# Kernel optimization log

Measured on AMD Instinct MI355X. Metric: run time of the kernel, lower is better.

## Reference

```python
import jax, jax.numpy as jnp
import numpy as np

B, P, E, D, A, M, V, L = 128, 196, 2048, 512, 512, 512, 10000, 21


def setup_inputs() -> dict:
    key = jax.random.key(0)
    ks = jax.random.split(key, 24)
    s = 0.02
    encoder_out = jax.random.normal(ks[0], (B, P, E), jnp.float32)
    encoded_captions = jax.random.randint(ks[1], (B, L), 0, V)
    caption_lengths = jax.random.randint(ks[2], (B,), 2, L + 1).at[0].set(L)
    return {
        "encoder_out": encoder_out,
        "encoded_captions": encoded_captions,
        "caption_lengths": caption_lengths,
        "emb_table": jax.random.normal(ks[3], (V, M), jnp.float32) * s,
        "enc_att_w": jax.random.normal(ks[4], (E, A), jnp.float32) * s,
        "enc_att_b": jnp.zeros((A,), jnp.float32),
        "dec_att_w": jax.random.normal(ks[5], (D, A), jnp.float32) * s,
        "dec_att_b": jnp.zeros((A,), jnp.float32),
        "full_att_w": jax.random.normal(ks[6], (A,), jnp.float32) * s,
        "full_att_b": jnp.zeros((), jnp.float32),
        "init_h_w": jax.random.normal(ks[7], (E, D), jnp.float32) * s,
        "init_h_b": jnp.zeros((D,), jnp.float32),
        "init_c_w": jax.random.normal(ks[8], (E, D), jnp.float32) * s,
        "init_c_b": jnp.zeros((D,), jnp.float32),
        "f_beta_w": jax.random.normal(ks[9], (D, E), jnp.float32) * s,
        "f_beta_b": jnp.zeros((E,), jnp.float32),
        "lstm_w_ih": jax.random.normal(ks[10], (4 * D, M + E), jnp.float32) * s,
        "lstm_b_ih": jnp.zeros((4 * D,), jnp.float32),
        "lstm_w_hh": jax.random.normal(ks[11], (4 * D, D), jnp.float32) * s,
        "lstm_b_hh": jnp.zeros((4 * D,), jnp.float32),
        "fc_w": jax.random.normal(ks[12], (V, D), jnp.float32) * s,
        "fc_b": jnp.zeros((V,), jnp.float32),
    }


def reference(encoder_out, encoded_captions, caption_lengths, emb_table,
              enc_att_w, enc_att_b, dec_att_w, dec_att_b, full_att_w, full_att_b,
              init_h_w, init_h_b, init_c_w, init_c_b, f_beta_w, f_beta_b,
              lstm_w_ih, lstm_b_ih, lstm_w_hh, lstm_b_hh, fc_w, fc_b):
    # sort by caption length descending (as in torch)
    order = jnp.argsort(-caption_lengths)
    enc = encoder_out[order]                 # [B,P,E]
    caps = encoded_captions[order]           # [B,L]
    dec_len = caption_lengths[order] - 1     # [B]
    T = caps.shape[1] - 1

    emb_seq = emb_table[caps]                # [B,L,M]
    mean = enc.mean(axis=1)                  # [B,E]
    h0 = mean @ init_h_w + init_h_b
    c0 = mean @ init_c_w + init_c_b
    att1 = enc @ enc_att_w + enc_att_b       # [B,P,A] (hoisted: constant over t)

    def step(carry, t):
        h, c = carry
        att2 = h @ dec_att_w + dec_att_b                              # [B,A]
        e = jnp.einsum('bpa,a->bp', jax.nn.relu(att1 + att2[:, None, :]), full_att_w) + full_att_b
        alpha = jax.nn.softmax(e, axis=1)                             # [B,P]
        awe = jnp.einsum('bpe,bp->be', enc, alpha)                    # [B,E]
        gate = jax.nn.sigmoid(h @ f_beta_w + f_beta_b)                # [B,E]
        x = jnp.concatenate([emb_seq[:, t, :], gate * awe], axis=1)   # [B,M+E]
        g = x @ lstm_w_ih.T + lstm_b_ih + h @ lstm_w_hh.T + lstm_b_hh
        i, f, gg, o = jnp.split(g, 4, axis=1)
        c_new = jax.nn.sigmoid(f) * c + jax.nn.sigmoid(i) * jnp.tanh(gg)
        h_new = jax.nn.sigmoid(o) * jnp.tanh(c_new)
        pred = h_new @ fc_w.T + fc_b                                  # [B,V]
        active = (t < dec_len)[:, None]
        pred = jnp.where(active, pred, 0.0)
        alpha = jnp.where(active, alpha, 0.0)
        return (h_new, c_new), (pred, alpha)

    _, (preds, alphas) = jax.lax.scan(step, (h0, c0), jnp.arange(T))
    predictions = jnp.moveaxis(preds, 0, 1)   # [B,T,V]
    alphas = jnp.moveaxis(alphas, 0, 1)       # [B,T,P]
    return predictions, alphas
```

## Files before the change

kernel.cpp:

```cpp
#include <hip/hip_runtime.h>
#include <math.h>

#define B_ 128
#define P_ 196
#define E_ 2048
#define D_ 512
#define A_ 512
#define M_ 512
#define V_ 10000
#define L_ 21
#define T_ 20

#define NBLK_ 256
#define SLOTS_WORDS (NBLK_ * 16 + 16)

typedef __attribute__((ext_vector_type(8))) short bf16x8;
typedef __attribute__((ext_vector_type(4))) float f32x4;
typedef unsigned short ushort_t;

__global__ void order_kernel(const int* __restrict__ lens, const int* __restrict__ caps,
                             int* __restrict__ order, int* __restrict__ declen,
                             int* __restrict__ row_map, int* __restrict__ tok_rows,
                             unsigned* __restrict__ bar) {
  __shared__ int s_order[B_];
  int tid = threadIdx.x;
  for (int i = tid; i < SLOTS_WORDS; i += 256) bar[i] = 0u;
  if (tid < B_) {
    int li = lens[tid];
    int r = 0;
    for (int j = 0; j < B_; ++j) {
      int lj = lens[j];
      r += (lj > li) || (lj == li && j < tid);
    }
    s_order[r] = tid;
    declen[r] = li - 1;
  }
  __syncthreads();
  if (tid < B_) order[tid] = s_order[tid];
  for (int m = tid; m < B_ * P_; m += blockDim.x) {
    int b = m / P_, p = m - b * P_;
    row_map[m] = s_order[b] * P_ + p;
  }
  for (int i = tid; i < T_ * B_; i += blockDim.x) {
    int t = i >> 7, b = i & 127;
    tok_rows[i] = caps[s_order[b] * L_ + t];
  }
}

__global__ void mean_kernel(const float* __restrict__ enc, const int* __restrict__ order,
                            float* __restrict__ mean) {
  int b = blockIdx.y;
  int e = blockIdx.x * blockDim.x + threadIdx.x;
  int ob = order[b];
  const float* base = enc + (long long)ob * P_ * E_ + e;
  float s = 0.f;
  for (int p = 0; p < P_; ++p) s += base[(long long)p * E_];
  mean[b * E_ + e] = s * (1.0f / P_);
}

__device__ __forceinline__ unsigned f2bf_u(float f) {
  unsigned u = __float_as_uint(f);
  return (u + 0x7fffu + ((u >> 16) & 1u)) >> 16;
}
__device__ __forceinline__ float bf2f(ushort_t h) {
  return __uint_as_float(((unsigned)h) << 16);
}

__global__ void enc2bf_kernel(const float* __restrict__ enc, const int* __restrict__ row_map,
                              ushort_t* __restrict__ out) {
  int r = blockIdx.x;
  int row = row_map[r];
  const float* src = enc + (long long)row * E_ + threadIdx.x * 8;
  float4 v0 = ((const float4*)src)[0];
  float4 v1 = ((const float4*)src)[1];
  float f[8] = {v0.x, v0.y, v0.z, v0.w, v1.x, v1.y, v1.z, v1.w};
  unsigned h[8];
#pragma unroll
  for (int j = 0; j < 8; ++j) h[j] = f2bf_u(f[j]);
  int4 o;
  o.x = (int)(h[0] | (h[1] << 16));
  o.y = (int)(h[2] | (h[3] << 16));
  o.z = (int)(h[4] | (h[5] << 16));
  o.w = (int)(h[6] | (h[7] << 16));
  *(int4*)(out + (long long)r * E_ + threadIdx.x * 8) = o;
}

__global__ void transpose_kernel(const float* __restrict__ in, float* __restrict__ out,
                                 int K, int N) {
  __shared__ float tt[32][33];
  int bx = blockIdx.x * 32;
  int by = blockIdx.y * 32;
  int lx = threadIdx.x & 31, ly = threadIdx.x >> 5;
#pragma unroll
  for (int i = 0; i < 32; i += 8) tt[ly + i][lx] = in[(long long)(by + ly + i) * N + bx + lx];
  __syncthreads();
#pragma unroll
  for (int i = 0; i < 32; i += 8)
    out[(long long)(bx + ly + i) * K + by + lx] = tt[lx][ly + i];
}

__global__ __launch_bounds__(256) void gemm32_kernel(
    const float* __restrict__ A, const float* __restrict__ Bm,
    const float* __restrict__ bias, float* __restrict__ C, int M, int N, int K) {
  __shared__ float As[16][64];
  __shared__ float Bs[16][64];
  const int tid = threadIdx.x;
  const int bm = blockIdx.y * 64, bn = blockIdx.x * 64;
  const int tm = tid >> 4, tn = tid & 15;
  float acc[4][4];
#pragma unroll
  for (int i = 0; i < 4; ++i)
#pragma unroll
    for (int j = 0; j < 4; ++j) acc[i][j] = 0.f;
  const int lm = tid >> 2;
  const int lk = (tid & 3) * 4;
  for (int k0 = 0; k0 < K; k0 += 16) {
    {
      int m = bm + lm;
      float4 v = make_float4(0.f, 0.f, 0.f, 0.f);
      if (m < M) v = *(const float4*)(A + (long long)m * K + k0 + lk);
      As[lk + 0][lm] = v.x;
      As[lk + 1][lm] = v.y;
      As[lk + 2][lm] = v.z;
      As[lk + 3][lm] = v.w;
    }
    {
      int k = tid >> 4;
      int n4 = (tid & 15) * 4;
      int n = bn + n4;
      float4 v = make_float4(0.f, 0.f, 0.f, 0.f);
      if (n < N) v = *(const float4*)(Bm + (long long)(k0 + k) * N + n);
      Bs[k][n4 + 0] = v.x;
      Bs[k][n4 + 1] = v.y;
      Bs[k][n4 + 2] = v.z;
      Bs[k][n4 + 3] = v.w;
    }
    __syncthreads();
#pragma unroll
    for (int k = 0; k < 16; ++k) {
      float a0 = As[k][tm * 4 + 0], a1 = As[k][tm * 4 + 1];
      float a2 = As[k][tm * 4 + 2], a3 = As[k][tm * 4 + 3];
      float b0 = Bs[k][tn * 4 + 0], b1 = Bs[k][tn * 4 + 1];
      float b2 = Bs[k][tn * 4 + 2], b3 = Bs[k][tn * 4 + 3];
      acc[0][0] += a0 * b0; acc[0][1] += a0 * b1; acc[0][2] += a0 * b2; acc[0][3] += a0 * b3;
      acc[1][0] += a1 * b0; acc[1][1] += a1 * b1; acc[1][2] += a1 * b2; acc[1][3] += a1 * b3;
      acc[2][0] += a2 * b0; acc[2][1] += a2 * b1; acc[2][2] += a2 * b2; acc[2][3] += a2 * b3;
      acc[3][0] += a3 * b0; acc[3][1] += a3 * b1; acc[3][2] += a3 * b2; acc[3][3] += a3 * b3;
    }
    __syncthreads();
  }
#pragma unroll
  for (int i = 0; i < 4; ++i) {
    int m = bm + tm * 4 + i;
    if (m >= M) continue;
#pragma unroll
    for (int j = 0; j < 4; ++j) {
      int n = bn + tn * 4 + j;
      if (n >= N) continue;
      C[(long long)m * N + n] = acc[i][j] + (bias ? bias[n] : 0.f);
    }
  }
}

__device__ __forceinline__ void stage16(short* __restrict__ Ph, short* __restrict__ Pl,
                                        int r, int kq, float4 v0, float4 v1, float4 v2,
                                        float4 v3, bool split) {
  float f[16] = {v0.x, v0.y, v0.z, v0.w, v1.x, v1.y, v1.z, v1.w,
                 v2.x, v2.y, v2.z, v2.w, v3.x, v3.y, v3.z, v3.w};
#pragma unroll
  for (int g2 = 0; g2 < 2; ++g2) {
    int gg = (kq >> 3) + g2;
    int slot = gg ^ ((r >> 1) & 3);
    unsigned hb[8];
    float lf[8];
#pragma unroll
    for (int j = 0; j < 8; ++j) {
      float x = f[g2 * 8 + j];
      hb[j] = f2bf_u(x);
      lf[j] = x - __uint_as_float(hb[j] << 16);
    }
    int4 ph;
    ph.x = (int)(hb[0] | (hb[1] << 16));
    ph.y = (int)(hb[2] | (hb[3] << 16));
    ph.z = (int)(hb[4] | (hb[5] << 16));
    ph.w = (int)(hb[6] | (hb[7] << 16));
    *(int4*)&Ph[r * 32 + slot * 8] = ph;
    if (split) {
      unsigned lb[8];
#pragma unroll
      for (int j = 0; j < 8; ++j) lb[j] = f2bf_u(lf[j]);
      int4 pl;
      pl.x = (int)(lb[0] | (lb[1] << 16));
      pl.y = (int)(lb[2] | (lb[3] << 16));
      pl.z = (int)(lb[4] | (lb[5] << 16));
      pl.w = (int)(lb[6] | (lb[7] << 16));
      *(int4*)&Pl[r * 32 + slot * 8] = pl;
    }
  }
}

__device__ __forceinline__ void stage8(short* __restrict__ Ph, short* __restrict__ Pl,
                                       int r, int kq8, float4 v0, float4 v1) {
  int slot = kq8 ^ ((r >> 1) & 3);
  float f[8] = {v0.x, v0.y, v0.z, v0.w, v1.x, v1.y, v1.z, v1.w};
  unsigned hb[8];
  float lf[8];
#pragma unroll
  for (int j = 0; j < 8; ++j) {
    hb[j] = f2bf_u(f[j]);
    lf[j] = f[j] - __uint_as_float(hb[j] << 16);
  }
  int4 ph;
  ph.x = (int)(hb[0] | (hb[1] << 16));
  ph.y = (int)(hb[2] | (hb[3] << 16));
  ph.z = (int)(hb[4] | (hb[5] << 16));
  ph.w = (int)(hb[6] | (hb[7] << 16));
  *(int4*)&Ph[r * 32 + slot * 8] = ph;
  unsigned lb[8];
#pragma unroll
  for (int j = 0; j < 8; ++j) lb[j] = f2bf_u(lf[j]);
  int4 pl;
  pl.x = (int)(lb[0] | (lb[1] << 16));
  pl.y = (int)(lb[2] | (lb[3] << 16));
  pl.z = (int)(lb[4] | (lb[5] << 16));
  pl.w = (int)(lb[6] | (lb[7] << 16));
  *(int4*)&Pl[r * 32 + slot * 8] = pl;
}

__device__ __forceinline__ bf16x8 frag_load(const short* __restrict__ P, int row, int g) {
  int slot = g ^ ((row >> 1) & 3);
  return *(const bf16x8*)&P[row * 32 + slot * 8];
}

template <int MODE, bool SPLIT, bool SWZ, bool OB>
__global__ __launch_bounds__(256) void mfma_gemm(
    const float* __restrict__ A, int lda, const int* __restrict__ row_map,
    const float* __restrict__ Bn, int ldb,
    const float* __restrict__ bias, const float* __restrict__ bias2,
    void* __restrict__ Cv, int ldc, int M, int N, int K,
    const int* __restrict__ declen) {
  __shared__ short Ah[128 * 32];
  __shared__ short Bh[128 * 32];
  __shared__ short Al[128 * 32];
  __shared__ short Bl[128 * 32];
  const int tid = threadIdx.x;
  int bxi, byi;
  if (SWZ) {
    int gx = gridDim.x, gy = gridDim.y;
    int id = blockIdx.y * gx + blockIdx.x;
    int super = 8 * gx;
    int body = (gy & ~7) * gx;
    if (id < body) {
      int s = id / super, rem = id % super;
      byi = s * 8 + (rem & 7);
      bxi = rem >> 3;
    } else {
      int rem = id - body;
      byi = (gy & ~7) + rem / gx;
      bxi = rem % gx;
    }
  } else {
    bxi = blockIdx.x;
    byi = blockIdx.y;
  }
  const int bm = byi * 128, bn = bxi * 128;

  f32x4 acc[4][4];
#pragma unroll
  for (int i = 0; i < 4; ++i)
#pragma unroll
    for (int j = 0; j < 4; ++j) acc[i][j] = (f32x4){0.f, 0.f, 0.f, 0.f};

  const int r = tid >> 1;
  const int kq = (tid & 1) * 16;
  const int am = bm + r;
  const long long arow = row_map ? (long long)row_map[am] : (long long)am;
  const float* ap = A + arow * (long long)lda + kq;
  const int gn = bn + r;
  const float* bp = Bn + (long long)gn * ldb + kq;
  const bool bok = gn < N;

  const int lane = tid & 63;
  const int wv = tid >> 6, wr = wv >> 1, wc = wv & 1;
  const int lr = lane & 15, g = lane >> 4;

  float4 z4 = make_float4(0.f, 0.f, 0.f, 0.f);
  float4 a0 = *(const float4*)(ap), a1 = *(const float4*)(ap + 4);
  float4 a2 = *(const float4*)(ap + 8), a3 = *(const float4*)(ap + 12);
  float4 b0 = bok ? *(const float4*)(bp) : z4;
  float4 b1 = bok ? *(const float4*)(bp + 4) : z4;
  float4 b2 = bok ? *(const float4*)(bp + 8) : z4;
  float4 b3 = bok ? *(const float4*)(bp + 12) : z4;

  for (int k0 = 0; k0 < K; k0 += 32) {
    stage16(Ah, Al, r, kq, a0, a1, a2, a3, SPLIT);
    stage16(Bh, Bl, r, kq, b0, b1, b2, b3, SPLIT);
    __syncthreads();
    if (k0 + 32 < K) {
      int kn = k0 + 32;
      a0 = *(const float4*)(ap + kn);
      a1 = *(const float4*)(ap + kn + 4);
      a2 = *(const float4*)(ap + kn + 8);
      a3 = *(const float4*)(ap + kn + 12);
      b0 = bok ? *(const float4*)(bp + kn) : z4;
      b1 = bok ? *(const float4*)(bp + kn + 4) : z4;
      b2 = bok ? *(const float4*)(bp + kn + 8) : z4;
      b3 = bok ? *(const float4*)(bp + kn + 12) : z4;
    }
    bf16x8 ah[4], bh[4];
#pragma unroll
    for (int i = 0; i < 4; ++i) {
      ah[i] = frag_load(Ah, wr * 64 + i * 16 + lr, g);
      bh[i] = frag_load(Bh, wc * 64 + i * 16 + lr, g);
    }
#pragma unroll
    for (int i = 0; i < 4; ++i)
#pragma unroll
      for (int j = 0; j < 4; ++j)
        acc[i][j] = __builtin_amdgcn_mfma_f32_16x16x32_bf16(ah[i], bh[j], acc[i][j], 0, 0, 0);
    if (SPLIT) {
      bf16x8 al2[4], bl2[4];
#pragma unroll
      for (int i = 0; i < 4; ++i) {
        al2[i] = frag_load(Al, wr * 64 + i * 16 + lr, g);
        bl2[i] = frag_load(Bl, wc * 64 + i * 16 + lr, g);
      }
#pragma unroll
      for (int i = 0; i < 4; ++i)
#pragma unroll
        for (int j = 0; j < 4; ++j)
          acc[i][j] = __builtin_amdgcn_mfma_f32_16x16x32_bf16(al2[i], bh[j], acc[i][j], 0, 0, 0);
#pragma unroll
      for (int i = 0; i < 4; ++i)
#pragma unroll
        for (int j = 0; j < 4; ++j)
          acc[i][j] = __builtin_amdgcn_mfma_f32_16x16x32_bf16(ah[i], bl2[j], acc[i][j], 0, 0, 0);
    }
    __syncthreads();
  }

#pragma unroll
  for (int j = 0; j < 4; ++j) {
    int n = bn + wc * 64 + j * 16 + lr;
    float bj = 0.f;
    if (n < N) {
      if (bias) bj += bias[n];
      if (bias2) bj += bias2[n];
    }
#pragma unroll
    for (int i = 0; i < 4; ++i) {
#pragma unroll
      for (int rr = 0; rr < 4; ++rr) {
        int m = bm + wr * 64 + i * 16 + g * 4 + rr;
        float v = acc[i][j][rr] + bj;
        if (MODE == 0) {
          if (OB)
            ((ushort_t*)Cv)[(long long)m * ldc + n] = (ushort_t)f2bf_u(v);
          else
            ((float*)Cv)[(long long)m * ldc + n] = v;
        } else {
          if (n < N) {
            int b = m & 127, t = m >> 7;
            ((float*)Cv)[(long long)b * (T_ * V_) + (long long)t * V_ + n] =
                (t < declen[b]) ? v : 0.f;
          }
        }
      }
    }
  }
}

__device__ __forceinline__ void mfma_tile64(
    const float* __restrict__ ap, const float* __restrict__ bp, int K,
    f32x4 (&acc)[2][2], short* Ah, short* Al, short* Bh, short* Bl,
    int sr, int skq, int wr, int wc, int lr, int g) {
  float4 a0 = *(const float4*)(ap), a1 = *(const float4*)(ap + 4);
  float4 b0 = *(const float4*)(bp), b1 = *(const float4*)(bp + 4);
  for (int k0 = 0; k0 < K; k0 += 32) {
    stage8(Ah, Al, sr, skq, a0, a1);
    stage8(Bh, Bl, sr, skq, b0, b1);
    __syncthreads();
    if (k0 + 32 < K) {
      a0 = *(const float4*)(ap + k0 + 32);
      a1 = *(const float4*)(ap + k0 + 36);
      b0 = *(const float4*)(bp + k0 + 32);
      b1 = *(const float4*)(bp + k0 + 36);
    }
    bf16x8 fah[2], fbh[2], fal[2], fbl[2];
#pragma unroll
    for (int i = 0; i < 2; ++i) {
      fah[i] = frag_load(Ah, wr * 32 + i * 16 + lr, g);
      fal[i] = frag_load(Al, wr * 32 + i * 16 + lr, g);
      fbh[i] = frag_load(Bh, wc * 32 + i * 16 + lr, g);
      fbl[i] = frag_load(Bl, wc * 32 + i * 16 + lr, g);
    }
#pragma unroll
    for (int i = 0; i < 2; ++i)
#pragma unroll
      for (int j = 0; j < 2; ++j) {
        acc[i][j] = __builtin_amdgcn_mfma_f32_16x16x32_bf16(fah[i], fbh[j], acc[i][j], 0, 0, 0);
        acc[i][j] = __builtin_amdgcn_mfma_f32_16x16x32_bf16(fal[i], fbh[j], acc[i][j], 0, 0, 0);
        acc[i][j] = __builtin_amdgcn_mfma_f32_16x16x32_bf16(fah[i], fbl[j], acc[i][j], 0, 0, 0);
      }
    __syncthreads();
  }
}

__device__ __forceinline__ void gsync(unsigned* __restrict__ slots, unsigned target) {
  __syncthreads();
  if (threadIdx.x == 0) {
    __threadfence();
    __hip_atomic_store(&slots[blockIdx.x * 16], target, __ATOMIC_RELEASE,
                       __HIP_MEMORY_SCOPE_AGENT);
  }
  if (threadIdx.x < 64) {
#pragma unroll
    for (int k = 0; k < 4; ++k) {
      unsigned idx = ((unsigned)threadIdx.x * 4 + k) * 16;
      while (__hip_atomic_load(&slots[idx], __ATOMIC_ACQUIRE, __HIP_MEMORY_SCOPE_AGENT) <
             target) {
        __builtin_amdgcn_s_sleep(2);
      }
    }
    __threadfence();
  }
  __syncthreads();
}

template <bool ENCBF>
__global__ __launch_bounds__(256, 1) void loop_kernel(
    const float* __restrict__ att1f, const ushort_t* __restrict__ att1b,
    const float* __restrict__ encf, const ushort_t* __restrict__ encb,
    const int* __restrict__ order, const int* __restrict__ declen,
    const float* __restrict__ decT, const float* __restrict__ decb,
    const float* __restrict__ fbT, const float* __restrict__ fbb,
    const float* __restrict__ whh, const float* __restrict__ wih,
    const float* __restrict__ faw, const float* __restrict__ fab,
    const float* __restrict__ g_all, float* __restrict__ g_part,
    float* __restrict__ gh, float* __restrict__ h_all, float* __restrict__ c,
    float* __restrict__ xh, float* __restrict__ gate, float* __restrict__ att2,
    float* __restrict__ alphas_out, unsigned* __restrict__ bar) {
  __shared__ short Ah[64 * 32];
  __shared__ short Bh[64 * 32];
  __shared__ short Al[64 * 32];
  __shared__ short Bl[64 * 32];
  __shared__ float att2_s[512];
  __shared__ float w_s[512];
  __shared__ float e_s[P_];
  __shared__ float red[8];

  unsigned* slots = bar;
  unsigned tgt = 0;

  const int bid = blockIdx.x, tid = threadIdx.x;
  const int lane = tid & 63, wv = tid >> 6, wr = wv >> 1, wc = wv & 1;
  const int lr = lane & 15, g = lane >> 4;
  const int sr = tid >> 2, skq = tid & 3;

  const float fb0 = fab[0];
  float wr8[8];
  if (ENCBF) {
    const float4* wp = (const float4*)(faw + lane * 8);
#pragma unroll
    for (int q = 0; q < 2; ++q) {
      float4 v = wp[q];
      wr8[q * 4 + 0] = v.x;
      wr8[q * 4 + 1] = v.y;
      wr8[q * 4 + 2] = v.z;
      wr8[q * 4 + 3] = v.w;
    }
  }

  for (int t = 0; t < T_; ++t) {
    const float* h_cur = h_all + t * (B_ * D_);
    if (bid < 144) {
      int nt = bid % 72, mt = bid / 72;
      int bn = nt * 64;
      const float* Bb;
      if (bn < 512) Bb = decT + bn * 512;
      else if (bn < 2560) Bb = fbT + (bn - 512) * 512;
      else Bb = whh + (bn - 2560) * 512;
      f32x4 acc[2][2];
#pragma unroll
      for (int i = 0; i < 2; ++i)
#pragma unroll
        for (int j = 0; j < 2; ++j) acc[i][j] = (f32x4){0.f, 0.f, 0.f, 0.f};
      mfma_tile64(h_cur + (mt * 64 + sr) * 512 + skq * 8, Bb + sr * 512 + skq * 8, 512,
                  acc, Ah, Al, Bh, Bl, sr, skq, wr, wc, lr, g);
#pragma unroll
      for (int j = 0; j < 2; ++j) {
        int n = bn + wc * 32 + j * 16 + lr;
#pragma unroll
        for (int i = 0; i < 2; ++i) {
#pragma unroll
          for (int rr = 0; rr < 4; ++rr) {
            int m = mt * 64 + wr * 32 + i * 16 + g * 4 + rr;
            float v = acc[i][j][rr];
            if (bn < 512) {
              att2[m * 512 + n] = v + decb[n];
            } else if (bn < 2560) {
              int nc = n - 512;
              gate[m * 2048 + nc] = 1.f / (1.f + __expf(-(v + fbb[nc])));
            } else {
              gh[m * 2048 + (n - 2560)] = v;
            }
          }
        }
      }
    }
    gsync(slots, ++tgt);
    {
      const int b = bid & 127, half = bid >> 7;
      if (ENCBF) {
        float a2r[8];
        const float4* a2p = (const float4*)(att2 + b * 512 + lane * 8);
#pragma unroll
        for (int q = 0; q < 2; ++q) {
          float4 v = a2p[q];
          a2r[q * 4 + 0] = v.x;
          a2r[q * 4 + 1] = v.y;
          a2r[q * 4 + 2] = v.z;
          a2r[q * 4 + 3] = v.w;
        }
        const ushort_t* a1base = att1b + (long long)b * P_ * 512 + lane * 8;
        const bf16x8 zv = (bf16x8)(short)0;
        for (int p0 = wv; p0 < P_; p0 += 16) {
          int pA = p0, pB = p0 + 4, pC = p0 + 8, pD = p0 + 12;
          bf16x8 hA = (pA < P_) ? *(const bf16x8*)(a1base + (long long)pA * 512) : zv;
          bf16x8 hB = (pB < P_) ? *(const bf16x8*)(a1base + (long long)pB * 512) : zv;
          bf16x8 hC = (pC < P_) ? *(const bf16x8*)(a1base + (long long)pC * 512) : zv;
          bf16x8 hD = (pD < P_) ? *(const bf16x8*)(a1base + (long long)pD * 512) : zv;
          float sA = 0.f, sB = 0.f, sC = 0.f, sD = 0.f;
#pragma unroll
          for (int j = 0; j < 8; ++j) {
            float xA = bf2f((ushort_t)hA[j]) + a2r[j];
            float xB = bf2f((ushort_t)hB[j]) + a2r[j];
            float xC = bf2f((ushort_t)hC[j]) + a2r[j];
            float xD = bf2f((ushort_t)hD[j]) + a2r[j];
            sA += (xA > 0.f ? xA : 0.f) * wr8[j];
            sB += (xB > 0.f ? xB : 0.f) * wr8[j];
            sC += (xC > 0.f ? xC : 0.f) * wr8[j];
            sD += (xD > 0.f ? xD : 0.f) * wr8[j];
          }
#pragma unroll
          for (int off = 32; off; off >>= 1) {
            sA += __shfl_down(sA, off);
            sB += __shfl_down(sB, off);
            sC += __shfl_down(sC, off);
            sD += __shfl_down(sD, off);
          }
          if (lane == 0) {
            e_s[pA] = sA + fb0;
            if (pB < P_) e_s[pB] = sB + fb0;
            if (pC < P_) e_s[pC] = sC + fb0;
            if (pD < P_) e_s[pD] = sD + fb0;
          }
        }
      } else {
        for (int i = tid; i < 512; i += 256) {
          att2_s[i] = att2[b * 512 + i];
          w_s[i] = faw[i];
        }
        __syncthreads();
        for (int p = wv; p < P_; p += 4) {
          const float* row = att1f + ((long long)b * P_ + p) * 512;
          float s = 0.f;
#pragma unroll
          for (int i2 = 0; i2 < 8; ++i2) {
            int ix = lane + i2 * 64;
            float v = row[ix] + att2_s[ix];
            s += (v > 0.f ? v : 0.f) * w_s[ix];
          }
          for (int off = 32; off; off >>= 1) s += __shfl_down(s, off);
          if (lane == 0) e_s[p] = s + fb0;
        }
      }
      __syncthreads();
      float mx = -1e30f;
      for (int p = tid; p < P_; p += 256) mx = fmaxf(mx, e_s[p]);
      for (int off = 32; off; off >>= 1) mx = fmaxf(mx, __shfl_down(mx, off));
      if (lane == 0) red[wv] = mx;
      __syncthreads();
      mx = fmaxf(fmaxf(red[0], red[1]), fmaxf(red[2], red[3]));
      float ssum = 0.f;
      for (int p = tid; p < P_; p += 256) {
        float ev = __expf(e_s[p] - mx);
        e_s[p] = ev;
        ssum += ev;
      }
      for (int off = 32; off; off >>= 1) ssum += __shfl_down(ssum, off);
      if (lane == 0) red[4 + wv] = ssum;
      __syncthreads();
      float inv = 1.f / (red[4] + red[5] + red[6] + red[7]);
      const bool active = (t < declen[b]);
      for (int p = tid; p < P_; p += 256) {
        float al = e_s[p] * inv;
        e_s[p] = al;
        if (half == 0)
          alphas_out[(long long)b * (T_ * P_) + t * P_ + p] = active ? al : 0.f;
      }
      __syncthreads();
      if (ENCBF) {
        const ushort_t* ebc = encb + (long long)b * (P_ * E_) + half * 1024 + tid * 4;
        int col = half * 1024 + tid * 4;
        float s0 = 0.f, s1 = 0.f, s2 = 0.f, s3 = 0.f;
        short4 buf0, buf1, buf2, buf3, buf4, buf5, buf6, buf7;
        buf0 = *(const short4*)(ebc + 0LL * E_);
        buf1 = *(const short4*)(ebc + 1LL * E_);
        buf2 = *(const short4*)(ebc + 2LL * E_);
        buf3 = *(const short4*)(ebc + 3LL * E_);
        buf4 = *(const short4*)(ebc + 4LL * E_);
        buf5 = *(const short4*)(ebc + 5LL * E_);
        buf6 = *(const short4*)(ebc + 6LL * E_);
        buf7 = *(const short4*)(ebc + 7LL * E_);
        for (int p0 = 0; p0 < 184; p0 += 8) {
          short4 c0 = buf0, c1 = buf1, c2 = buf2, c3 = buf3;
          short4 c4 = buf4, c5 = buf5, c6 = buf6, c7 = buf7;
          const ushort_t* nb = ebc + (long long)(p0 + 8) * E_;
          buf0 = *(const short4*)(nb + 0LL * E_);
          buf1 = *(const short4*)(nb + 1LL * E_);
          buf2 = *(const short4*)(nb + 2LL * E_);
          buf3 = *(const short4*)(nb + 3LL * E_);
          buf4 = *(const short4*)(nb + 4LL * E_);
          buf5 = *(const short4*)(nb + 5LL * E_);
          buf6 = *(const short4*)(nb + 6LL * E_);
          buf7 = *(const short4*)(nb + 7LL * E_);
          float a;
          a = e_s[p0 + 0]; s0 += a * bf2f((ushort_t)c0.x); s1 += a * bf2f((ushort_t)c0.y); s2 += a * bf2f((ushort_t)c0.z); s3 += a * bf2f((ushort_t)c0.w);
          a = e_s[p0 + 1]; s0 += a * bf2f((ushort_t)c1.x); s1 += a * bf2f((ushort_t)c1.y); s2 += a * bf2f((ushort_t)c1.z); s3 += a * bf2f((ushort_t)c1.w);
          a = e_s[p0 + 2]; s0 += a * bf2f((ushort_t)c2.x); s1 += a * bf2f((ushort_t)c2.y); s2 += a * bf2f((ushort_t)c2.z); s3 += a * bf2f((ushort_t)c2.w);
          a = e_s[p0 + 3]; s0 += a * bf2f((ushort_t)c3.x); s1 += a * bf2f((ushort_t)c3.y); s2 += a * bf2f((ushort_t)c3.z); s3 += a * bf2f((ushort_t)c3.w);
          a = e_s[p0 + 4]; s0 += a * bf2f((ushort_t)c4.x); s1 += a * bf2f((ushort_t)c4.y); s2 += a * bf2f((ushort_t)c4.z); s3 += a * bf2f((ushort_t)c4.w);
          a = e_s[p0 + 5]; s0 += a * bf2f((ushort_t)c5.x); s1 += a * bf2f((ushort_t)c5.y); s2 += a * bf2f((ushort_t)c5.z); s3 += a * bf2f((ushort_t)c5.w);
          a = e_s[p0 + 6]; s0 += a * bf2f((ushort_t)c6.x); s1 += a * bf2f((ushort_t)c6.y); s2 += a * bf2f((ushort_t)c6.z); s3 += a * bf2f((ushort_t)c6.w);
          a = e_s[p0 + 7]; s0 += a * bf2f((ushort_t)c7.x); s1 += a * bf2f((ushort_t)c7.y); s2 += a * bf2f((ushort_t)c7.z); s3 += a * bf2f((ushort_t)c7.w);
        }
        {
          float a;
          a = e_s[184]; s0 += a * bf2f((ushort_t)buf0.x); s1 += a * bf2f((ushort_t)buf0.y); s2 += a * bf2f((ushort_t)buf0.z); s3 += a * bf2f((ushort_t)buf0.w);
          a = e_s[185]; s0 += a * bf2f((ushort_t)buf1.x); s1 += a * bf2f((ushort_t)buf1.y); s2 += a * bf2f((ushort_t)buf1.z); s3 += a * bf2f((ushort_t)buf1.w);
          a = e_s[186]; s0 += a * bf2f((ushort_t)buf2.x); s1 += a * bf2f((ushort_t)buf2.y); s2 += a * bf2f((ushort_t)buf2.z); s3 += a * bf2f((ushort_t)buf2.w);
          a = e_s[187]; s0 += a * bf2f((ushort_t)buf3.x); s1 += a * bf2f((ushort_t)buf3.y); s2 += a * bf2f((ushort_t)buf3.z); s3 += a * bf2f((ushort_t)buf3.w);
          a = e_s[188]; s0 += a * bf2f((ushort_t)buf4.x); s1 += a * bf2f((ushort_t)buf4.y); s2 += a * bf2f((ushort_t)buf4.z); s3 += a * bf2f((ushort_t)buf4.w);
          a = e_s[189]; s0 += a * bf2f((ushort_t)buf5.x); s1 += a * bf2f((ushort_t)buf5.y); s2 += a * bf2f((ushort_t)buf5.z); s3 += a * bf2f((ushort_t)buf5.w);
          a = e_s[190]; s0 += a * bf2f((ushort_t)buf6.x); s1 += a * bf2f((ushort_t)buf6.y); s2 += a * bf2f((ushort_t)buf6.z); s3 += a * bf2f((ushort_t)buf6.w);
          a = e_s[191]; s0 += a * bf2f((ushort_t)buf7.x); s1 += a * bf2f((ushort_t)buf7.y); s2 += a * bf2f((ushort_t)buf7.z); s3 += a * bf2f((ushort_t)buf7.w);
          short4 t0 = *(const short4*)(ebc + 192LL * E_);
          short4 t1 = *(const short4*)(ebc + 193LL * E_);
          short4 t2 = *(const short4*)(ebc + 194LL * E_);
          short4 t3 = *(const short4*)(ebc + 195LL * E_);
          a = e_s[192]; s0 += a * bf2f((ushort_t)t0.x); s1 += a * bf2f((ushort_t)t0.y); s2 += a * bf2f((ushort_t)t0.z); s3 += a * bf2f((ushort_t)t0.w);
          a = e_s[193]; s0 += a * bf2f((ushort_t)t1.x); s1 += a * bf2f((ushort_t)t1.y); s2 += a * bf2f((ushort_t)t1.z); s3 += a * bf2f((ushort_t)t1.w);
          a = e_s[194]; s0 += a * bf2f((ushort_t)t2.x); s1 += a * bf2f((ushort_t)t2.y); s2 += a * bf2f((ushort_t)t2.z); s3 += a * bf2f((ushort_t)t2.w);
          a = e_s[195]; s0 += a * bf2f((ushort_t)t3.x); s1 += a * bf2f((ushort_t)t3.y); s2 += a * bf2f((ushort_t)t3.z); s3 += a * bf2f((ushort_t)t3.w);
        }
        float4 gv = *(const float4*)(gate + b * 2048 + col);
        float4 o;
        o.x = gv.x * s0;
        o.y = gv.y * s1;
        o.z = gv.z * s2;
        o.w = gv.w * s3;
        *(float4*)(xh + b * 2048 + col) = o;
      } else {
        const int ob = order[b];
        const float* eb = encf + (long long)ob * (P_ * E_);
        for (int e0 = half * 1024 + tid; e0 < half * 1024 + 1024; e0 += 256) {
          float s2 = 0.f;
#pragma unroll 4
          for (int p = 0; p < P_; ++p) s2 += e_s[p] * eb[p * 2048 + e0];
          xh[b * 2048 + e0] = gate[b * 2048 + e0] * s2;
        }
      }
    }
    gsync(slots, ++tgt);
    {
      int kc = bid >> 6, rem = bid & 63, mt = rem >> 5, nt = rem & 31;
      int bn = nt * 64;
      f32x4 acc[2][2];
#pragma unroll
      for (int i = 0; i < 2; ++i)
#pragma unroll
        for (int j = 0; j < 2; ++j) acc[i][j] = (f32x4){0.f, 0.f, 0.f, 0.f};
      mfma_tile64(xh + (mt * 64 + sr) * 2048 + kc * 512 + skq * 8,
                  wih + (long long)(bn + sr) * 2560 + 512 + kc * 512 + skq * 8, 512,
                  acc, Ah, Al, Bh, Bl, sr, skq, wr, wc, lr, g);
      float* gp = g_part + kc * (128 * 2048);
#pragma unroll
      for (int j = 0; j < 2; ++j) {
        int n = bn + wc * 32 + j * 16 + lr;
#pragma unroll
        for (int i = 0; i < 2; ++i) {
#pragma unroll
          for (int rr = 0; rr < 4; ++rr) {
            int m = mt * 64 + wr * 32 + i * 16 + g * 4 + rr;
            gp[m * 2048 + n] = acc[i][j][rr];
          }
        }
      }
    }
    gsync(slots, ++tgt);
    {
      int idx = bid * 256 + tid;
      int b = idx >> 9, d = idx & 511;
      int base = b * 2048 + d;
      const float* ge = g_all + (long long)t * (128 * 2048);
      float gi = ge[base] + gh[base];
      float gf2 = ge[base + 512] + gh[base + 512];
      float gg2 = ge[base + 1024] + gh[base + 1024];
      float go = ge[base + 1536] + gh[base + 1536];
#pragma unroll
      for (int kc = 0; kc < 4; ++kc) {
        const float* gp = g_part + kc * (128 * 2048) + base;
        gi += gp[0];
        gf2 += gp[512];
        gg2 += gp[1024];
        go += gp[1536];
      }
      float si = 1.f / (1.f + __expf(-gi));
      float sf = 1.f / (1.f + __expf(-gf2));
      float so = 1.f / (1.f + __expf(-go));
      float cn = sf * c[idx] + si * tanhf(gg2);
      float hn = so * tanhf(cn);
      c[idx] = cn;
      h_all[(t + 1) * (B_ * D_) + idx] = hn;
    }
    gsync(slots, ++tgt);
  }
}

extern "C" void kernel_launch(void* const* d_in, const int* in_sizes, int n_in,
                              void* d_out, int out_size, void* d_ws, size_t ws_size,
                              hipStream_t stream) {
  const float* enc       = (const float*)d_in[0];
  const int*   caps      = (const int*)d_in[1];
  const int*   lens      = (const int*)d_in[2];
  const float* emb       = (const float*)d_in[3];
  const float* enc_att_w = (const float*)d_in[4];
  const float* enc_att_b = (const float*)d_in[5];
  const float* dec_att_w = (const float*)d_in[6];
  const float* dec_att_b = (const float*)d_in[7];
  const float* full_att_w = (const float*)d_in[8];
  const float* full_att_b = (const float*)d_in[9];
  const float* init_h_w  = (const float*)d_in[10];
  const float* init_h_b  = (const float*)d_in[11];
  const float* init_c_w  = (const float*)d_in[12];
  const float* init_c_b  = (const float*)d_in[13];
  const float* f_beta_w  = (const float*)d_in[14];
  const float* f_beta_b  = (const float*)d_in[15];
  const float* lstm_w_ih = (const float*)d_in[16];
  const float* lstm_b_ih = (const float*)d_in[17];
  const float* lstm_w_hh = (const float*)d_in[18];
  const float* lstm_b_hh = (const float*)d_in[19];
  const float* fc_w      = (const float*)d_in[20];
  const float* fc_b      = (const float*)d_in[21];

  float* out = (float*)d_out;
  float* alphas_out = out + (long long)B_ * T_ * V_;

  float* g_all    = out;
  float* g_part   = out + 6 * 1024 * 1024;
  float* encattwT = out + 8 * 1024 * 1024;
  float* decT     = out + 9 * 1024 * 1024 + 512 * 1024;
  float* fbT      = decT + 512 * 512;
  float* gh       = out + 12 * 1024 * 1024;

  size_t cur = 0;
  char* wsb = (char*)d_ws;
  auto alloc = [&](size_t bytes) {
    size_t off = cur;
    cur = (cur + bytes + 255) & ~(size_t)255;
    return (void*)(wsb + off);
  };
  const size_t ATT1B_BYTES = (size_t)B_ * P_ * A_ * 2;
  const size_t ENCB_BYTES  = (size_t)B_ * P_ * E_ * 2;
  const size_t ATT1F_BYTES = (size_t)B_ * P_ * A_ * 4;
  const size_t REST_BYTES  = (size_t)(B_ * E_ + (T_ + 1) * B_ * D_ + B_ * D_ + B_ * A_ +
                                      B_ * E_ + B_ * E_) * 4 +
                             (2 * B_ + B_ * P_ + T_ * B_ + SLOTS_WORDS + 64) * 4 + 4096;
  const bool bfpath = ws_size >= ATT1B_BYTES + ENCB_BYTES + REST_BYTES + (1u << 20);

  ushort_t* att1b = nullptr;
  ushort_t* encbf = nullptr;
  float* att1f = nullptr;
  if (bfpath) {
    att1b = (ushort_t*)alloc(ATT1B_BYTES);
    encbf = (ushort_t*)alloc(ENCB_BYTES);
  } else {
    att1f = (float*)alloc(ATT1F_BYTES);
  }
  float* mean  = (float*)alloc((size_t)B_ * E_ * 4);
  float* h_all = (float*)alloc((size_t)(T_ + 1) * B_ * D_ * 4);
  float* c     = (float*)alloc((size_t)B_ * D_ * 4);
  float* att2  = (float*)alloc((size_t)B_ * A_ * 4);
  float* gate  = (float*)alloc((size_t)B_ * E_ * 4);
  float* xh    = (float*)alloc((size_t)B_ * E_ * 4);
  int* order   = (int*)alloc(B_ * 4);
  int* declen  = (int*)alloc(B_ * 4);
  int* row_map = (int*)alloc((size_t)B_ * P_ * 4);
  int* tok_rows = (int*)alloc((size_t)T_ * B_ * 4);
  unsigned* bar = (unsigned*)alloc(SLOTS_WORDS * 4);

  hipLaunchKernelGGL(order_kernel, dim3(1), dim3(256), 0, stream, lens, caps, order, declen,
                     row_map, tok_rows, bar);
  hipLaunchKernelGGL(transpose_kernel, dim3(16, 64), dim3(256), 0, stream, enc_att_w,
                     encattwT, E_, A_);
  hipLaunchKernelGGL(transpose_kernel, dim3(16, 16), dim3(256), 0, stream, dec_att_w, decT,
                     D_, A_);
  hipLaunchKernelGGL(transpose_kernel, dim3(64, 16), dim3(256), 0, stream, f_beta_w, fbT,
                     D_, E_);
  hipLaunchKernelGGL(mean_kernel, dim3(E_ / 256, B_), dim3(256), 0, stream, enc, order, mean);
  hipLaunchKernelGGL(gemm32_kernel, dim3(D_ / 64, 2), dim3(256), 0, stream, mean, init_h_w,
                     init_h_b, h_all, B_, D_, E_);
  hipLaunchKernelGGL(gemm32_kernel, dim3(D_ / 64, 2), dim3(256), 0, stream, mean, init_c_w,
                     init_c_b, c, B_, D_, E_);
  if (bfpath) {
    hipLaunchKernelGGL((mfma_gemm<0, false, true, true>), dim3(A_ / 128, (B_ * P_) / 128),
                       dim3(256), 0, stream, enc, E_, row_map, encattwT, E_, enc_att_b,
                       (const float*)nullptr, (void*)att1b, A_, B_ * P_, A_, E_,
                       (const int*)nullptr);
    hipLaunchKernelGGL(enc2bf_kernel, dim3(B_ * P_), dim3(256), 0, stream, enc, row_map,
                       encbf);
  } else {
    hipLaunchKernelGGL((mfma_gemm<0, false, true, false>), dim3(A_ / 128, (B_ * P_) / 128),
                       dim3(256), 0, stream, enc, E_, row_map, encattwT, E_, enc_att_b,
                       (const float*)nullptr, (void*)att1f, A_, B_ * P_, A_, E_,
                       (const int*)nullptr);
  }
  hipLaunchKernelGGL((mfma_gemm<0, true, false, false>), dim3((4 * D_) / 128, (T_ * B_) / 128),
                     dim3(256), 0, stream, emb, M_, tok_rows, lstm_w_ih, M_ + E_, lstm_b_ih,
                     lstm_b_hh, (void*)g_all, 4 * D_, T_ * B_, 4 * D_, M_,
                     (const int*)nullptr);
  if (bfpath) {
    hipLaunchKernelGGL((loop_kernel<true>), dim3(NBLK_), dim3(256), 0, stream,
                       (const float*)nullptr, att1b, (const float*)nullptr, encbf, order,
                       declen, decT, dec_att_b, fbT, f_beta_b, lstm_w_hh, lstm_w_ih,
                       full_att_w, full_att_b, g_all, g_part, gh, h_all, c, xh, gate, att2,
                       alphas_out, bar);
  } else {
    hipLaunchKernelGGL((loop_kernel<false>), dim3(NBLK_), dim3(256), 0, stream, att1f,
                       (const ushort_t*)nullptr, enc, (const ushort_t*)nullptr, order,
                       declen, decT, dec_att_b, fbT, f_beta_b, lstm_w_hh, lstm_w_ih,
                       full_att_w, full_att_b, g_all, g_part, gh, h_all, c, xh, gate, att2,
                       alphas_out, bar);
  }
  hipLaunchKernelGGL((mfma_gemm<1, true, false, false>), dim3((V_ + 127) / 128,
                     (T_ * B_) / 128), dim3(256), 0, stream, h_all + B_ * D_, D_,
                     (const int*)nullptr, fc_w, D_, fc_b, (const float*)nullptr, (void*)out,
                     V_, T_ * B_, V_, D_, declen);
}
```

Measured before the change: 5.078 ms.

## Double persistent loop grid to 512 blocks with quarter-column attention-weighted sums

```diff
diff --git a/kernel.cpp b/kernel.cpp
--- a/kernel.cpp
+++ b/kernel.cpp
@@ -11,8 +11,8 @@
 #define L_ 21
 #define T_ 20
 
-#define NBLK_ 256
-#define SLOTS_WORDS (NBLK_ * 16 + 16)
+#define NBLK_ 512
+#define SLOTS_WORDS (NBLK_ * 16 + NBLK_ * 16 + 16)
 
 typedef __attribute__((ext_vector_type(8))) short bf16x8;
 typedef __attribute__((ext_vector_type(4))) float f32x4;
@@ -415,8 +415,8 @@
   }
   if (threadIdx.x < 64) {
 #pragma unroll
-    for (int k = 0; k < 4; ++k) {
-      unsigned idx = ((unsigned)threadIdx.x * 4 + k) * 16;
+    for (int k = 0; k < NBLK_ / 64; ++k) {
+      unsigned idx = ((unsigned)threadIdx.x * (NBLK_ / 64) + k) * 16;
       while (__hip_atomic_load(&slots[idx], __ATOMIC_ACQUIRE, __HIP_MEMORY_SCOPE_AGENT) <
              target) {
         __builtin_amdgcn_s_sleep(2);
@@ -428,7 +428,7 @@
 }
 
 template <bool ENCBF>
-__global__ __launch_bounds__(256, 1) void loop_kernel(
+__global__ __launch_bounds__(256, 2) void loop_kernel(
     const float* __restrict__ att1f, const ushort_t* __restrict__ att1b,
     const float* __restrict__ encf, const ushort_t* __restrict__ encb,
     const int* __restrict__ order, const int* __restrict__ declen,
@@ -439,7 +439,8 @@
     const float* __restrict__ g_all, float* __restrict__ g_part,
     float* __restrict__ gh, float* __restrict__ h_all, float* __restrict__ c,
     float* __restrict__ xh, float* __restrict__ gate, float* __restrict__ att2,
-    float* __restrict__ alphas_out, unsigned* __restrict__ bar) {
+    float* __restrict__ alphas_out, unsigned* __restrict__ bar,
+    float* __restrict__ e_g) {
   __shared__ short Ah[64 * 32];
   __shared__ short Bh[64 * 32];
   __shared__ short Al[64 * 32];
@@ -450,6 +451,7 @@
   __shared__ float red[8];
 
   unsigned* slots = bar;
+  unsigned* pf = bar + NBLK_ * 16;
   unsigned tgt = 0;
 
   const int bid = blockIdx.x, tid = threadIdx.x;
@@ -510,165 +512,187 @@
     }
     gsync(slots, ++tgt);
     {
-      const int b = bid & 127, half = bid >> 7;
+      const int b = bid & 127, q = bid >> 7;
       if (ENCBF) {
-        float a2r[8];
-        const float4* a2p = (const float4*)(att2 + b * 512 + lane * 8);
-#pragma unroll
-        for (int q = 0; q < 2; ++q) {
-          float4 v = a2p[q];
-          a2r[q * 4 + 0] = v.x;
-          a2r[q * 4 + 1] = v.y;
-          a2r[q * 4 + 2] = v.z;
-          a2r[q * 4 + 3] = v.w;
+        if (q < 2) {
+          float a2r[8];
+          const float4* a2p = (const float4*)(att2 + b * 512 + lane * 8);
+#pragma unroll
+          for (int qq = 0; qq < 2; ++qq) {
+            float4 v = a2p[qq];
+            a2r[qq * 4 + 0] = v.x;
+            a2r[qq * 4 + 1] = v.y;
+            a2r[qq * 4 + 2] = v.z;
+            a2r[qq * 4 + 3] = v.w;
+          }
+          const ushort_t* a1base = att1b + (long long)b * P_ * 512 + lane * 8;
+          const bf16x8 zv = (bf16x8)(short)0;
+          for (int p0 = wv; p0 < P_; p0 += 16) {
+            int pA = p0, pB = p0 + 4, pC = p0 + 8, pD = p0 + 12;
+            bf16x8 hA = (pA < P_) ? *(const bf16x8*)(a1base + (long long)pA * 512) : zv;
+            bf16x8 hB = (pB < P_) ? *(const bf16x8*)(a1base + (long long)pB * 512) : zv;
+            bf16x8 hC = (pC < P_) ? *(const bf16x8*)(a1base + (long long)pC * 512) : zv;
+            bf16x8 hD = (pD < P_) ? *(const bf16x8*)(a1base + (long long)pD * 512) : zv;
+            float sA = 0.f, sB = 0.f, sC = 0.f, sD = 0.f;
+#pragma unroll
+            for (int j = 0; j < 8; ++j) {
+              float xA = bf2f((ushort_t)hA[j]) + a2r[j];
+              float xB = bf2f((ushort_t)hB[j]) + a2r[j];
+              float xC = bf2f((ushort_t)hC[j]) + a2r[j];
+              float xD = bf2f((ushort_t)hD[j]) + a2r[j];
+              sA += (xA > 0.f ? xA : 0.f) * wr8[j];
+              sB += (xB > 0.f ? xB : 0.f) * wr8[j];
+              sC += (xC > 0.f ? xC : 0.f) * wr8[j];
+              sD += (xD > 0.f ? xD : 0.f) * wr8[j];
+            }
+#pragma unroll
+            for (int off = 32; off; off >>= 1) {
+              sA += __shfl_down(sA, off);
+              sB += __shfl_down(sB, off);
+              sC += __shfl_down(sC, off);
+              sD += __shfl_down(sD, off);
+            }
+            if (lane == 0) {
+              e_s[pA] = sA + fb0;
+              if (pB < P_) e_s[pB] = sB + fb0;
+              if (pC < P_) e_s[pC] = sC + fb0;
+              if (pD < P_) e_s[pD] = sD + fb0;
+            }
+          }
+          __syncthreads();
+          float mx = -1e30f;
+          for (int p = tid; p < P_; p += 256) mx = fmaxf(mx, e_s[p]);
+          for (int off = 32; off; off >>= 1) mx = fmaxf(mx, __shfl_down(mx, off));
+          if (lane == 0) red[wv] = mx;
+          __syncthreads();
+          mx = fmaxf(fmaxf(red[0], red[1]), fmaxf(red[2], red[3]));
+          float ssum = 0.f;
+          for (int p = tid; p < P_; p += 256) {
+            float ev = __expf(e_s[p] - mx);
+            e_s[p] = ev;
+            ssum += ev;
+          }
+          for (int off = 32; off; off >>= 1) ssum += __shfl_down(ssum, off);
+          if (lane == 0) red[4 + wv] = ssum;
+          __syncthreads();
+          float inv = 1.f / (red[4] + red[5] + red[6] + red[7]);
+          const bool active = (t < declen[b]);
+          for (int p = tid; p < P_; p += 256) {
+            float al = e_s[p] * inv;
+            e_s[p] = al;
+            if (q == 0) {
+              alphas_out[(long long)b * (T_ * P_) + t * P_ + p] = active ? al : 0.f;
+              e_g[b * 256 + p] = al;
+            }
+          }
+          __syncthreads();
+          if (q == 0 && tid == 0) {
+            __threadfence();
+            __hip_atomic_store(&pf[b * 16], (unsigned)(t + 1), __ATOMIC_RELEASE,
+                               __HIP_MEMORY_SCOPE_AGENT);
+          }
+        } else {
+          if (tid == 0) {
+            while (__hip_atomic_load(&pf[b * 16], __ATOMIC_ACQUIRE,
+                                     __HIP_MEMORY_SCOPE_AGENT) < (unsigned)(t + 1)) {
+              __builtin_amdgcn_s_sleep(2);
+            }
+            __threadfence();
+          }
+          __syncthreads();
+          for (int p = tid; p < P_; p += 256) e_s[p] = e_g[b * 256 + p];
+          __syncthreads();
         }
-        const ushort_t* a1base = att1b + (long long)b * P_ * 512 + lane * 8;
-        const bf16x8 zv = (bf16x8)(short)0;
-        for (int p0 = wv; p0 < P_; p0 += 16) {
-          int pA = p0, pB = p0 + 4, pC = p0 + 8, pD = p0 + 12;
-          bf16x8 hA = (pA < P_) ? *(const bf16x8*)(a1base + (long long)pA * 512) : zv;
-          bf16x8 hB = (pB < P_) ? *(const bf16x8*)(a1base + (long long)pB * 512) : zv;
-          bf16x8 hC = (pC < P_) ? *(const bf16x8*)(a1base + (long long)pC * 512) : zv;
-          bf16x8 hD = (pD < P_) ? *(const bf16x8*)(a1base + (long long)pD * 512) : zv;
-          float sA = 0.f, sB = 0.f, sC = 0.f, sD = 0.f;
-#pragma unroll
-          for (int j = 0; j < 8; ++j) {
-            float xA = bf2f((ushort_t)hA[j]) + a2r[j];
-            float xB = bf2f((ushort_t)hB[j]) + a2r[j];
-            float xC = bf2f((ushort_t)hC[j]) + a2r[j];
-            float xD = bf2f((ushort_t)hD[j]) + a2r[j];
-            sA += (xA > 0.f ? xA : 0.f) * wr8[j];
-            sB += (xB > 0.f ? xB : 0.f) * wr8[j];
-            sC += (xC > 0.f ? xC : 0.f) * wr8[j];
-            sD += (xD > 0.f ? xD : 0.f) * wr8[j];
-          }
-#pragma unroll
-          for (int off = 32; off; off >>= 1) {
-            sA += __shfl_down(sA, off);
-            sB += __shfl_down(sB, off);
-            sC += __shfl_down(sC, off);
-            sD += __shfl_down(sD, off);
-          }
-          if (lane == 0) {
-            e_s[pA] = sA + fb0;
-            if (pB < P_) e_s[pB] = sB + fb0;
-            if (pC < P_) e_s[pC] = sC + fb0;
-            if (pD < P_) e_s[pD] = sD + fb0;
-          }
+        {
+          const int col = q * 512 + tid * 2;
+          const ushort_t* ebc = encb + (long long)b * (P_ * E_) + col;
+          float s0 = 0.f, s1 = 0.f;
+          short2 buf[14];
+#pragma unroll
+          for (int i = 0; i < 14; ++i) buf[i] = *(const short2*)(ebc + (long long)i * E_);
+          for (int ch = 0; ch < 13; ++ch) {
+            short2 cur[14];
+#pragma unroll
+            for (int i = 0; i < 14; ++i) cur[i] = buf[i];
+            const ushort_t* nb = ebc + (long long)(ch + 1) * 14 * E_;
+#pragma unroll
+            for (int i = 0; i < 14; ++i) buf[i] = *(const short2*)(nb + (long long)i * E_);
+            const float* ep = e_s + ch * 14;
+#pragma unroll
+            for (int i = 0; i < 14; ++i) {
+              float a = ep[i];
+              s0 += a * bf2f((ushort_t)cur[i].x);
+              s1 += a * bf2f((ushort_t)cur[i].y);
+            }
+          }
+          {
+            const float* ep = e_s + 182;
+#pragma unroll
+            for (int i = 0; i < 14; ++i) {
+              float a = ep[i];
+              s0 += a * bf2f((ushort_t)buf[i].x);
+              s1 += a * bf2f((ushort_t)buf[i].y);
+            }
+          }
+          float2 gv = *(const float2*)(gate + b * 2048 + col);
+          float2 o;
+          o.x = gv.x * s0;
+          o.y = gv.y * s1;
+          *(float2*)(xh + b * 2048 + col) = o;
         }
       } else {
-        for (int i = tid; i < 512; i += 256) {
-          att2_s[i] = att2[b * 512 + i];
-          w_s[i] = faw[i];
-        }
-        __syncthreads();
-        for (int p = wv; p < P_; p += 4) {
-          const float* row = att1f + ((long long)b * P_ + p) * 512;
-          float s = 0.f;
-#pragma unroll
-          for (int i2 = 0; i2 < 8; ++i2) {
-            int ix = lane + i2 * 64;
-            float v = row[ix] + att2_s[ix];
-            s += (v > 0.f ? v : 0.f) * w_s[ix];
-          }
-          for (int off = 32; off; off >>= 1) s += __shfl_down(s, off);
-          if (lane == 0) e_s[p] = s + fb0;
-        }
-      }
-      __syncthreads();
-      float mx = -1e30f;
-      for (int p = tid; p < P_; p += 256) mx = fmaxf(mx, e_s[p]);
-      for (int off = 32; off; off >>= 1) mx = fmaxf(mx, __shfl_down(mx, off));
-      if (lane == 0) red[wv] = mx;
-      __syncthreads();
-      mx = fmaxf(fmaxf(red[0], red[1]), fmaxf(red[2], red[3]));
-      float ssum = 0.f;
-      for (int p = tid; p < P_; p += 256) {
-        float ev = __expf(e_s[p] - mx);
-        e_s[p] = ev;
-        ssum += ev;
-      }
-      for (int off = 32; off; off >>= 1) ssum += __shfl_down(ssum, off);
-      if (lane == 0) red[4 + wv] = ssum;
-      __syncthreads();
-      float inv = 1.f / (red[4] + red[5] + red[6] + red[7]);
-      const bool active = (t < declen[b]);
-      for (int p = tid; p < P_; p += 256) {
-        float al = e_s[p] * inv;
-        e_s[p] = al;
-        if (half == 0)
-          alphas_out[(long long)b * (T_ * P_) + t * P_ + p] = active ? al : 0.f;
-      }
-      __syncthreads();
-      if (ENCBF) {
-        const ushort_t* ebc = encb + (long long)b * (P_ * E_) + half * 1024 + tid * 4;
-        int col = half * 1024 + tid * 4;
-        float s0 = 0.f, s1 = 0.f, s2 = 0.f, s3 = 0.f;
-        short4 buf0, buf1, buf2, buf3, buf4, buf5, buf6, buf7;
-        buf0 = *(const short4*)(ebc + 0LL * E_);
-        buf1 = *(const short4*)(ebc + 1LL * E_);
-        buf2 = *(const short4*)(ebc + 2LL * E_);
-        buf3 = *(const short4*)(ebc + 3LL * E_);
-        buf4 = *(const short4*)(ebc + 4LL * E_);
-        buf5 = *(const short4*)(ebc + 5LL * E_);
-        buf6 = *(const short4*)(ebc + 6LL * E_);
-        buf7 = *(const short4*)(ebc + 7LL * E_);
-        for (int p0 = 0; p0 < 184; p0 += 8) {
-          short4 c0 = buf0, c1 = buf1, c2 = buf2, c3 = buf3;
-          short4 c4 = buf4, c5 = buf5, c6 = buf6, c7 = buf7;
-          const ushort_t* nb = ebc + (long long)(p0 + 8) * E_;
-          buf0 = *(const short4*)(nb + 0LL * E_);
-          buf1 = *(const short4*)(nb + 1LL * E_);
-          buf2 = *(const short4*)(nb + 2LL * E_);
-          buf3 = *(const short4*)(nb + 3LL * E_);
-          buf4 = *(const short4*)(nb + 4LL * E_);
-          buf5 = *(const short4*)(nb + 5LL * E_);
-          buf6 = *(const short4*)(nb + 6LL * E_);
-          buf7 = *(const short4*)(nb + 7LL * E_);
-          float a;
-          a = e_s[p0 + 0]; s0 += a * bf2f((ushort_t)c0.x); s1 += a * bf2f((ushort_t)c0.y); s2 += a * bf2f((ushort_t)c0.z); s3 += a * bf2f((ushort_t)c0.w);
-          a = e_s[p0 + 1]; s0 += a * bf2f((ushort_t)c1.x); s1 += a * bf2f((ushort_t)c1.y); s2 += a * bf2f((ushort_t)c1.z); s3 += a * bf2f((ushort_t)c1.w);
-          a = e_s[p0 + 2]; s0 += a * bf2f((ushort_t)c2.x); s1 += a * bf2f((ushort_t)c2.y); s2 += a * bf2f((ushort_t)c2.z); s3 += a * bf2f((ushort_t)c2.w);
-          a = e_s[p0 + 3]; s0 += a * bf2f((ushort_t)c3.x); s1 += a * bf2f((ushort_t)c3.y); s2 += a * bf2f((ushort_t)c3.z); s3 += a * bf2f((ushort_t)c3.w);
-          a = e_s[p0 + 4]; s0 += a * bf2f((ushort_t)c4.x); s1 += a * bf2f((ushort_t)c4.y); s2 += a * bf2f((ushort_t)c4.z); s3 += a * bf2f((ushort_t)c4.w);
-          a = e_s[p0 + 5]; s0 += a * bf2f((ushort_t)c5.x); s1 += a * bf2f((ushort_t)c5.y); s2 += a * bf2f((ushort_t)c5.z); s3 += a * bf2f((ushort_t)c5.w);
-          a = e_s[p0 + 6]; s0 += a * bf2f((ushort_t)c6.x); s1 += a * bf2f((ushort_t)c6.y); s2 += a * bf2f((ushort_t)c6.z); s3 += a * bf2f((ushort_t)c6.w);
-          a = e_s[p0 + 7]; s0 += a * bf2f((ushort_t)c7.x); s1 += a * bf2f((ushort_t)c7.y); s2 += a * bf2f((ushort_t)c7.z); s3 += a * bf2f((ushort_t)c7.w);
-        }
-        {
-          float a;
-          a = e_s[184]; s0 += a * bf2f((ushort_t)buf0.x); s1 += a * bf2f((ushort_t)buf0.y); s2 += a * bf2f((ushort_t)buf0.z); s3 += a * bf2f((ushort_t)buf0.w);
-          a = e_s[185]; s0 += a * bf2f((ushort_t)buf1.x); s1 += a * bf2f((ushort_t)buf1.y); s2 += a * bf2f((ushort_t)buf1.z); s3 += a * bf2f((ushort_t)buf1.w);
-          a = e_s[186]; s0 += a * bf2f((ushort_t)buf2.x); s1 += a * bf2f((ushort_t)buf2.y); s2 += a * bf2f((ushort_t)buf2.z); s3 += a * bf2f((ushort_t)buf2.w);
-          a = e_s[187]; s0 += a * bf2f((ushort_t)buf3.x); s1 += a * bf2f((ushort_t)buf3.y); s2 += a * bf2f((ushort_t)buf3.z); s3 += a * bf2f((ushort_t)buf3.w);
-          a = e_s[188]; s0 += a * bf2f((ushort_t)buf4.x); s1 += a * bf2f((ushort_t)buf4.y); s2 += a * bf2f((ushort_t)buf4.z); s3 += a * bf2f((ushort_t)buf4.w);
-          a = e_s[189]; s0 += a * bf2f((ushort_t)buf5.x); s1 += a * bf2f((ushort_t)buf5.y); s2 += a * bf2f((ushort_t)buf5.z); s3 += a * bf2f((ushort_t)buf5.w);
-          a = e_s[190]; s0 += a * bf2f((ushort_t)buf6.x); s1 += a * bf2f((ushort_t)buf6.y); s2 += a * bf2f((ushort_t)buf6.z); s3 += a * bf2f((ushort_t)buf6.w);
-          a = e_s[191]; s0 += a * bf2f((ushort_t)buf7.x); s1 += a * bf2f((ushort_t)buf7.y); s2 += a * bf2f((ushort_t)buf7.z); s3 += a * bf2f((ushort_t)buf7.w);
-          short4 t0 = *(const short4*)(ebc + 192LL * E_);
-          short4 t1 = *(const short4*)(ebc + 193LL * E_);
-          short4 t2 = *(const short4*)(ebc + 194LL * E_);
-          short4 t3 = *(const short4*)(ebc + 195LL * E_);
-          a = e_s[192]; s0 += a * bf2f((ushort_t)t0.x); s1 += a * bf2f((ushort_t)t0.y); s2 += a * bf2f((ushort_t)t0.z); s3 += a * bf2f((ushort_t)t0.w);
-          a = e_s[193]; s0 += a * bf2f((ushort_t)t1.x); s1 += a * bf2f((ushort_t)t1.y); s2 += a * bf2f((ushort_t)t1.z); s3 += a * bf2f((ushort_t)t1.w);
-          a = e_s[194]; s0 += a * bf2f((ushort_t)t2.x); s1 += a * bf2f((ushort_t)t2.y); s2 += a * bf2f((ushort_t)t2.z); s3 += a * bf2f((ushort_t)t2.w);
-          a = e_s[195]; s0 += a * bf2f((ushort_t)t3.x); s1 += a * bf2f((ushort_t)t3.y); s2 += a * bf2f((ushort_t)t3.z); s3 += a * bf2f((ushort_t)t3.w);
-        }
-        float4 gv = *(const float4*)(gate + b * 2048 + col);
-        float4 o;
-        o.x = gv.x * s0;
-        o.y = gv.y * s1;
-        o.z = gv.z * s2;
-        o.w = gv.w * s3;
-        *(float4*)(xh + b * 2048 + col) = o;
-      } else {
-        const int ob = order[b];
-        const float* eb = encf + (long long)ob * (P_ * E_);
-        for (int e0 = half * 1024 + tid; e0 < half * 1024 + 1024; e0 += 256) {
-          float s2 = 0.f;
+        if (q < 2) {
+          const int half = q;
+          for (int i = tid; i < 512; i += 256) {
+            att2_s[i] = att2[b * 512 + i];
+            w_s[i] = faw[i];
+          }
+          __syncthreads();
+          for (int p = wv; p < P_; p += 4) {
+            const float* row = att1f + ((long long)b * P_ + p) * 512;
+            float s = 0.f;
+#pragma unroll
+            for (int i2 = 0; i2 < 8; ++i2) {
+              int ix = lane + i2 * 64;
+              float v = row[ix] + att2_s[ix];
+              s += (v > 0.f ? v : 0.f) * w_s[ix];
+            }
+            for (int off = 32; off; off >>= 1) s += __shfl_down(s, off);
+            if (lane == 0) e_s[p] = s + fb0;
+          }
+          __syncthreads();
+          float mx = -1e30f;
+          for (int p = tid; p < P_; p += 256) mx = fmaxf(mx, e_s[p]);
+          for (int off = 32; off; off >>= 1) mx = fmaxf(mx, __shfl_down(mx, off));
+          if (lane == 0) red[wv] = mx;
+          __syncthreads();
+          mx = fmaxf(fmaxf(red[0], red[1]), fmaxf(red[2], red[3]));
+          float ssum = 0.f;
+          for (int p = tid; p < P_; p += 256) {
+            float ev = __expf(e_s[p] - mx);
+            e_s[p] = ev;
+            ssum += ev;
+          }
+          for (int off = 32; off; off >>= 1) ssum += __shfl_down(ssum, off);
+          if (lane == 0) red[4 + wv] = ssum;
+          __syncthreads();
+          float inv = 1.f / (red[4] + red[5] + red[6] + red[7]);
+          const bool active = (t < declen[b]);
+          for (int p = tid; p < P_; p += 256) {
+            float al = e_s[p] * inv;
+            e_s[p] = al;
+            if (half == 0)
+              alphas_out[(long long)b * (T_ * P_) + t * P_ + p] = active ? al : 0.f;
+          }
+          __syncthreads();
+          const int ob = order[b];
+          const float* eb = encf + (long long)ob * (P_ * E_);
+          for (int e0 = half * 1024 + tid; e0 < half * 1024 + 1024; e0 += 256) {
+            float s2 = 0.f;
 #pragma unroll 4
-          for (int p = 0; p < P_; ++p) s2 += e_s[p] * eb[p * 2048 + e0];
-          xh[b * 2048 + e0] = gate[b * 2048 + e0] * s2;
+            for (int p = 0; p < P_; ++p) s2 += e_s[p] * eb[p * 2048 + e0];
+            xh[b * 2048 + e0] = gate[b * 2048 + e0] * s2;
+          }
         }
       }
     }
@@ -681,8 +705,8 @@
       for (int i = 0; i < 2; ++i)
 #pragma unroll
         for (int j = 0; j < 2; ++j) acc[i][j] = (f32x4){0.f, 0.f, 0.f, 0.f};
-      mfma_tile64(xh + (mt * 64 + sr) * 2048 + kc * 512 + skq * 8,
-                  wih + (long long)(bn + sr) * 2560 + 512 + kc * 512 + skq * 8, 512,
+      mfma_tile64(xh + (mt * 64 + sr) * 2048 + kc * 256 + skq * 8,
+                  wih + (long long)(bn + sr) * 2560 + 512 + kc * 256 + skq * 8, 256,
                   acc, Ah, Al, Bh, Bl, sr, skq, wr, wc, lr, g);
       float* gp = g_part + kc * (128 * 2048);
 #pragma unroll
@@ -699,7 +723,7 @@
       }
     }
     gsync(slots, ++tgt);
-    {
+    if (bid < 256) {
       int idx = bid * 256 + tid;
       int b = idx >> 9, d = idx & 511;
       int base = b * 2048 + d;
@@ -709,7 +733,7 @@
       float gg2 = ge[base + 1024] + gh[base + 1024];
       float go = ge[base + 1536] + gh[base + 1536];
 #pragma unroll
-      for (int kc = 0; kc < 4; ++kc) {
+      for (int kc = 0; kc < 8; ++kc) {
         const float* gp = g_part + kc * (128 * 2048) + base;
         gi += gp[0];
         gf2 += gp[512];
@@ -763,6 +787,7 @@
   float* decT     = out + 9 * 1024 * 1024 + 512 * 1024;
   float* fbT      = decT + 512 * 512;
   float* gh       = out + 12 * 1024 * 1024;
+  float* e_g      = out + 13 * 1024 * 1024;
 
   size_t cur = 0;
   char* wsb = (char*)d_ws;
@@ -835,13 +860,13 @@
                        (const float*)nullptr, att1b, (const float*)nullptr, encbf, order,
                        declen, decT, dec_att_b, fbT, f_beta_b, lstm_w_hh, lstm_w_ih,
                        full_att_w, full_att_b, g_all, g_part, gh, h_all, c, xh, gate, att2,
-                       alphas_out, bar);
+                       alphas_out, bar, e_g);
   } else {
     hipLaunchKernelGGL((loop_kernel<false>), dim3(NBLK_), dim3(256), 0, stream, att1f,
                        (const ushort_t*)nullptr, enc, (const ushort_t*)nullptr, order,
                        declen, decT, dec_att_b, fbT, f_beta_b, lstm_w_hh, lstm_w_ih,
                        full_att_w, full_att_b, g_all, g_part, gh, h_all, c, xh, gate, att2,
-                       alphas_out, bar);
+                       alphas_out, bar, e_g);
   }
   hipLaunchKernelGGL((mfma_gemm<1, true, false, false>), dim3((V_ + 127) / 128,
                      (T_ * B_) / 128), dim3(256), 0, stream, h_all + B_ * D_, D_,
```

Result: slower. 13.36 ms (+163.0%).
